# Kernel optimization log

Measured on AMD Instinct MI355X. Metric: run time of the kernel, lower is better.

Reference implementation:

```python
import jax, jax.numpy as jnp
import numpy as np

HEADS = 16
DIM_HEAD = 64
SCALE = DIM_HEAD ** -0.5
EPS = 1e-5


def _vdp_linear(mu, sigma, Wmu, Wsig_raw):
    # y = W x with W ~ N(Wmu, softplus(Wsig_raw)), x ~ N(mu, sigma) (diag covs):
    # Var(y) = (mu^2 + sigma) @ Wsig^T + sigma @ (Wmu^2)^T
    Wsig = jax.nn.softplus(Wsig_raw)
    mu_y = mu @ Wmu.T
    sigma_y = (mu * mu + sigma) @ Wsig.T + sigma @ (Wmu * Wmu).T
    return mu_y, sigma_y


def _vdp_layernorm(mu, sigma, gamma, beta):
    mean = jnp.mean(mu, axis=-1, keepdims=True)
    var = jnp.var(mu, axis=-1, keepdims=True)
    inv = 1.0 / jnp.sqrt(var + EPS)
    mu_y = (mu - mean) * inv * gamma + beta
    # first-order variance propagation through the affine normalization
    sigma_y = sigma * (gamma * gamma) * (inv * inv)
    return mu_y, sigma_y


def _vdp_softmax(mu, sigma):
    p = jax.nn.softmax(mu, axis=-1)
    # diagonal-Jacobian approximation: J_ii = p_i(1-p_i)
    J = p * (1.0 - p)
    return p, (J * J) * sigma


def setup_inputs() -> dict:
    key = jax.random.key(0)
    ks = jax.random.split(key, 6)
    B, N, D = 4, 1024, 1024
    inner = HEADS * DIM_HEAD  # 1024
    w_std = 0.02
    return {
        "mu": jax.random.normal(ks[0], (B, N, D), jnp.float32),
        "sigma": jax.random.uniform(ks[1], (B, N, D), jnp.float32),
        "ln_gamma": jnp.ones((D,), jnp.float32),
        "ln_beta": jnp.zeros((D,), jnp.float32),
        "Wqkv_mu": w_std * jax.random.normal(ks[2], (3 * inner, D), jnp.float32),
        "Wqkv_sigma_raw": -5.0 + 0.1 * jax.random.normal(ks[3], (3 * inner, D), jnp.float32),
        "Wout_mu": w_std * jax.random.normal(ks[4], (D, inner), jnp.float32),
        "Wout_sigma_raw": -5.0 + 0.1 * jax.random.normal(ks[5], (D, inner), jnp.float32),
    }


def reference(mu, sigma, ln_gamma, ln_beta, Wqkv_mu, Wqkv_sigma_raw, Wout_mu, Wout_sigma_raw):
    B, N, D = mu.shape

    mu_n, sigma_n = _vdp_layernorm(mu, sigma, ln_gamma, ln_beta)
    mu_qkv, sigma_qkv = _vdp_linear(mu_n, sigma_n, Wqkv_mu, Wqkv_sigma_raw)

    def split_heads(t):
        q, k, v = jnp.split(t, 3, axis=-1)
        rs = lambda a: a.reshape(B, N, HEADS, DIM_HEAD).transpose(0, 2, 1, 3)
        return rs(q), rs(k), rs(v)

    mu_q, mu_k, mu_v = split_heads(mu_qkv)
    sg_q, sg_k, sg_v = split_heads(sigma_qkv)

    mu_dots = jnp.einsum("bhid,bhjd->bhij", mu_q, mu_k) * SCALE
    sg_dots = jnp.einsum("bhid,bhjd->bhij", sg_q, sg_k) * SCALE

    mu_attn, sg_attn = _vdp_softmax(mu_dots, sg_dots)

    mu_o = jnp.einsum("bhij,bhjd->bhid", mu_attn, mu_v)
    sg_o = jnp.einsum("bhij,bhjd->bhid", sg_attn, sg_v)

    merge = lambda t: t.transpose(0, 2, 1, 3).reshape(B, N, HEADS * DIM_HEAD)
    mu_o, sg_o = merge(mu_o), merge(sg_o)

    return _vdp_linear(mu_o, sg_o, Wout_mu, Wout_sigma_raw)
```

## Files before the change

kernel.cpp:

```cpp
#include <hip/hip_runtime.h>

typedef unsigned short u16;
typedef unsigned int u32;
typedef __bf16 bf16x8 __attribute__((ext_vector_type(8)));
typedef float f32x4 __attribute__((ext_vector_type(4)));
typedef float f32x16 __attribute__((ext_vector_type(16)));

__device__ __forceinline__ float b2f(u16 u) { return __uint_as_float(((u32)u) << 16); }
__device__ __forceinline__ u16 f2b(float f) {
  u32 u = __float_as_uint(f);
  u += 0x7fffu + ((u >> 16) & 1u);
  return (u16)(u >> 16);
}

__device__ __forceinline__ void gll16(const u16* g, u16* l) {
  __builtin_amdgcn_global_load_lds(
      (const __attribute__((address_space(1))) void*)g,
      (__attribute__((address_space(3))) void*)l, 16, 0, 0);
}

__device__ __forceinline__ float4 load4(const void* p, size_t idx, bool f32) {
  if (f32) return *(const float4*)((const float*)p + idx);
  ushort4 u = *(const ushort4*)((const u16*)p + idx);
  return make_float4(b2f(u.x), b2f(u.y), b2f(u.z), b2f(u.w));
}

__global__ __launch_bounds__(256) void detect_kernel(const u16* __restrict__ sig,
                                                     int* __restrict__ flag) {
  __shared__ int cnt;
  if (threadIdx.x == 0) cnt = 0;
  __syncthreads();
  int c = 0;
  for (int i = threadIdx.x; i < 16384; i += 256) {
    u16 v = sig[i];
    c += ((v & 0x7F80u) == 0x7F80u) ? 1 : 0;
  }
  atomicAdd(&cnt, c);
  __syncthreads();
  if (threadIdx.x == 0) *flag = (cnt >= 8) ? 1 : 0;
}

__global__ __launch_bounds__(256) void ln_prep_kernel(
    const int* __restrict__ flag,
    const void* __restrict__ mu, const void* __restrict__ sigma,
    const void* __restrict__ gamma, const void* __restrict__ beta,
    u16* __restrict__ mu_n, u16* __restrict__ a1sg)
{
  __shared__ float ps[4], pq[4];
  const bool f32 = (*flag != 0);
  const int t = threadIdx.x;
  const int wv = t >> 6, lane = t & 63;
  const size_t base = (size_t)blockIdx.x * 1024 + (size_t)t * 4;
  float4 xm = load4(mu, base, f32);
  float4 xs = load4(sigma, base, f32);
  float x0 = xm.x, x1 = xm.y, x2 = xm.z, x3 = xm.w;
  float s0 = xs.x, s1 = xs.y, s2 = xs.z, s3 = xs.w;

  float sv = x0 + x1 + x2 + x3;
  float qv = x0*x0 + x1*x1 + x2*x2 + x3*x3;
  #pragma unroll
  for (int off = 32; off > 0; off >>= 1) {
    sv += __shfl_xor(sv, off, 64);
    qv += __shfl_xor(qv, off, 64);
  }
  if (lane == 0) { ps[wv] = sv; pq[wv] = qv; }
  __syncthreads();
  float sum = ps[0] + ps[1] + ps[2] + ps[3];
  float ssq = pq[0] + pq[1] + pq[2] + pq[3];

  float mean = sum * (1.0f / 1024.0f);
  float var  = ssq * (1.0f / 1024.0f) - mean * mean;
  float inv  = 1.0f / sqrtf(var + 1e-5f);
  float inv2 = inv * inv;

  float4 g4 = load4(gamma, (size_t)t * 4, f32);
  float4 b4 = load4(beta, (size_t)t * 4, f32);

  float m0 = (x0 - mean) * inv * g4.x + b4.x;
  float m1 = (x1 - mean) * inv * g4.y + b4.y;
  float m2 = (x2 - mean) * inv * g4.z + b4.z;
  float m3 = (x3 - mean) * inv * g4.w + b4.w;
  float v0 = s0 * g4.x * g4.x * inv2;
  float v1 = s1 * g4.y * g4.y * inv2;
  float v2 = s2 * g4.z * g4.z * inv2;
  float v3 = s3 * g4.w * g4.w * inv2;

  ushort4 omu = { f2b(m0), f2b(m1), f2b(m2), f2b(m3) };
  ushort4 oa1 = { f2b(m0*m0 + v0), f2b(m1*m1 + v1), f2b(m2*m2 + v2), f2b(m3*m3 + v3) };
  ushort4 osg = { f2b(v0), f2b(v1), f2b(v2), f2b(v3) };
  *(ushort4*)(mu_n + base) = omu;
  size_t r2 = (size_t)blockIdx.x * 2048 + (size_t)t * 4;
  *(ushort4*)(a1sg + r2) = oa1;
  *(ushort4*)(a1sg + r2 + 1024) = osg;
}

__global__ __launch_bounds__(256) void wprep_kernel(
    const int* __restrict__ flag,
    const void* __restrict__ wq_mu, const void* __restrict__ wq_sraw,
    u16* __restrict__ q_bf, u16* __restrict__ q_s2,
    const void* __restrict__ wo_mu, const void* __restrict__ wo_sraw,
    u16* __restrict__ o_bf, u16* __restrict__ o_s2, int nq)
{
  const bool f32 = (*flag != 0);
  size_t idx = ((size_t)blockIdx.x * 256 + threadIdx.x) * 4;
  const void *wmu, *wsr; u16 *obf, *os2;
  if (idx < (size_t)nq) { wmu = wq_mu; wsr = wq_sraw; obf = q_bf; os2 = q_s2; }
  else { idx -= nq; wmu = wo_mu; wsr = wo_sraw; obf = o_bf; os2 = o_s2; }
  int row = (int)(idx >> 10), k = (int)(idx & 1023);
  float4 m4 = load4(wmu, idx, f32);
  float4 s4 = load4(wsr, idx, f32);
  float m[4] = { m4.x, m4.y, m4.z, m4.w };
  float s[4] = { s4.x, s4.y, s4.z, s4.w };
  ushort4 ob, os, oq;
  u16* obp = (u16*)&ob; u16* osp = (u16*)&os; u16* oqp = (u16*)&oq;
  #pragma unroll
  for (int i = 0; i < 4; ++i) {
    float sp = (s[i] > 15.f) ? s[i] : log1pf(__expf(s[i]));
    obp[i] = f2b(m[i]);
    osp[i] = f2b(sp);
    oqp[i] = f2b(m[i] * m[i]);
  }
  *(ushort4*)(obf + idx) = ob;
  size_t r2 = (size_t)row * 2048 + k;
  *(ushort4*)(os2 + r2) = os;
  *(ushort4*)(os2 + r2 + 1024) = oq;
}

template<bool DYN>
__global__ __launch_bounds__(256, 4) void gemm_pair_kernel(
    const u16* __restrict__ A0, const u16* __restrict__ B0, int K0, void* C0, size_t ob0,
    const u16* __restrict__ A1, const u16* __restrict__ B1, int K1, void* C1, size_t ob1,
    int split, int N, const int* __restrict__ flag)
{
  __shared__ u16 lA[128 * 64];
  __shared__ u16 lB[128 * 64];
  const int t = threadIdx.x;
  int bx = blockIdx.x;
  const u16 *A, *B; void* C; size_t obase; int K;
  if (bx < split) { A = A0; B = B0; K = K0; C = C0; obase = ob0; }
  else { bx -= split; A = A1; B = B1; K = K1; C = C1; obase = ob1; }

  const int n0 = bx * 128, m0 = blockIdx.y * 128;
  const int lane = t & 63, wave = t >> 6;
  const int wr = (wave >> 1) * 64, wc = (wave & 1) * 64;
  const int m31 = lane & 31, h5 = lane >> 5;
  const int mx = m31 & 7;

  const int srow = t >> 3;
  const int gseg = (t & 7) ^ (srow & 7);

  f32x16 acc[2][2];
  #pragma unroll
  for (int i = 0; i < 2; ++i)
    #pragma unroll
    for (int j = 0; j < 2; ++j)
      #pragma unroll
      for (int r = 0; r < 16; ++r) acc[i][j][r] = 0.f;

  for (int k0 = 0; k0 < K; k0 += 64) {
    __syncthreads();
    #pragma unroll
    for (int rep = 0; rep < 4; ++rep) {
      gll16(A + (size_t)(m0 + srow + rep * 32) * K + k0 + gseg * 8,
            lA + rep * 2048 + wave * 512);
      gll16(B + (size_t)(n0 + srow + rep * 32) * K + k0 + gseg * 8,
            lB + rep * 2048 + wave * 512);
    }
    __syncthreads();
    #pragma unroll
    for (int ks = 0; ks < 4; ++ks) {
      const int seg = ks * 2 + h5;
      bf16x8 af[2], bfr[2];
      #pragma unroll
      for (int tm = 0; tm < 2; ++tm)
        af[tm] = *(const bf16x8*)&lA[(wr + tm * 32 + m31) * 64 + (seg ^ mx) * 8];
      #pragma unroll
      for (int tn = 0; tn < 2; ++tn)
        bfr[tn] = *(const bf16x8*)&lB[(wc + tn * 32 + m31) * 64 + (seg ^ mx) * 8];
      #pragma unroll
      for (int tm = 0; tm < 2; ++tm)
        #pragma unroll
        for (int tn = 0; tn < 2; ++tn)
          acc[tm][tn] = __builtin_amdgcn_mfma_f32_32x32x16_bf16(af[tm], bfr[tn], acc[tm][tn], 0, 0, 0);
    }
  }

  const bool of32 = DYN && (*flag != 0);
  #pragma unroll
  for (int tm = 0; tm < 2; ++tm)
    #pragma unroll
    for (int tn = 0; tn < 2; ++tn) {
      int colb = n0 + wc + tn * 32 + m31;
      #pragma unroll
      for (int r = 0; r < 16; ++r) {
        int row = m0 + wr + tm * 32 + (r & 3) + 8 * (r >> 2) + 4 * h5;
        float v = acc[tm][tn][r];
        size_t off = obase + (size_t)row * N + colb;
        if (DYN) {
          if (of32) ((float*)C)[off] = v;
          else      ((u16*)C)[off] = f2b(v);
        } else {
          ((u16*)C)[off] = f2b(v);
        }
      }
    }
}

__global__ __launch_bounds__(256) void attn_pass1(
    const u16* __restrict__ qkv_mu, float* __restrict__ invl)
{
  __shared__ u16 lK[128 * 72];
  const int t = threadIdx.x;
  const int wv = t >> 6, lane = t & 63;
  const int ml = lane & 15, qd = lane >> 4;
  const int bh = blockIdx.y;
  const int b = bh >> 4, h = bh & 15;
  const size_t rowbase = (size_t)b * 1024 * 3072;
  const int i0 = blockIdx.x * 64;
  const int qcol = h * 64, kcol = 1024 + h * 64;
  const int qrow = wv * 16;

  bf16x8 aQm[2];
  #pragma unroll
  for (int ks = 0; ks < 2; ++ks)
    aQm[ks] = *(const bf16x8*)(qkv_mu + rowbase +
        (size_t)(i0 + qrow + ml) * 3072 + qcol + ks * 32 + qd * 8);

  float lsum[4] = {0.f, 0.f, 0.f, 0.f};

  for (int j0 = 0; j0 < 1024; j0 += 128) {
    __syncthreads();
    #pragma unroll
    for (int rep = 0; rep < 4; ++rep) {
      int c = t + rep * 256;
      int row = c >> 3, seg = c & 7;
      *(uint4*)&lK[row * 72 + seg * 8] =
          *(const uint4*)(qkv_mu + rowbase + (size_t)(j0 + row) * 3072 + kcol + seg * 8);
    }
    __syncthreads();
    #pragma unroll
    for (int tj = 0; tj < 8; ++tj) {
      bf16x8 b0 = *(const bf16x8*)&lK[(tj * 16 + ml) * 72 + qd * 8];
      bf16x8 b1 = *(const bf16x8*)&lK[(tj * 16 + ml) * 72 + 32 + qd * 8];
      f32x4 s = (f32x4){0.f, 0.f, 0.f, 0.f};
      s = __builtin_amdgcn_mfma_f32_16x16x32_bf16(aQm[0], b0, s, 0, 0, 0);
      s = __builtin_amdgcn_mfma_f32_16x16x32_bf16(aQm[1], b1, s, 0, 0, 0);
      #pragma unroll
      for (int r = 0; r < 4; ++r) lsum[r] += __expf(s[r] * 0.125f);
    }
  }
  #pragma unroll
  for (int r = 0; r < 4; ++r) {
    float l = lsum[r];
    #pragma unroll
    for (int xo = 1; xo < 16; xo <<= 1) l += __shfl_xor(l, xo, 64);
    if (ml == 0)
      invl[(size_t)bh * 1024 + i0 + qrow + qd * 4 + r] = 1.0f / l;
  }
}

__global__ __launch_bounds__(512, 4) void attn_pass2(
    const u16* __restrict__ qkv_mu, const u16* __restrict__ qkv_sg,
    const float* __restrict__ invl,
    u16* __restrict__ o_mu, u16* __restrict__ a1sgo)
{
  __shared__ u16 lKW[128 * 72];
  __shared__ u16 lV[128 * 72];
  __shared__ u16 lP[128 * 72];
  __shared__ u16 lW[128 * 72];

  const int t = threadIdx.x;
  const int wv = t >> 6, lane = t & 63;
  const int ml = lane & 15, qd = lane >> 4;
  const int bh = blockIdx.y;
  const int b = bh >> 4, h = bh & 15;
  const size_t rowbase = (size_t)b * 1024 * 3072;
  const int i0 = blockIdx.x * 128;
  const int qcol = h * 64, kcol = 1024 + h * 64, vcol = 2048 + h * 64;
  const int qrow = wv * 16;

  bf16x8 aQm[2], aQs[2];
  #pragma unroll
  for (int ks = 0; ks < 2; ++ks) {
    size_t ga = rowbase + (size_t)(i0 + qrow + ml) * 3072 + qcol + ks * 32 + qd * 8;
    aQm[ks] = *(const bf16x8*)(qkv_mu + ga);
    aQs[ks] = *(const bf16x8*)(qkv_sg + ga);
  }

  float lacc[4];
  #pragma unroll
  for (int r = 0; r < 4; ++r)
    lacc[r] = invl[(size_t)bh * 1024 + i0 + qrow + qd * 4 + r];

  f32x4 accm[4], accs[4];
  #pragma unroll
  for (int tj = 0; tj < 4; ++tj) {
    accm[tj] = (f32x4){0.f, 0.f, 0.f, 0.f};
    accs[tj] = (f32x4){0.f, 0.f, 0.f, 0.f};
  }

  for (int j0 = 0; j0 < 1024; j0 += 64) {
    __syncthreads();
    #pragma unroll
    for (int rep = 0; rep < 2; ++rep) {
      int c = t + rep * 512;
      int row = c >> 3, seg = c & 7;
      const u16* src = (row < 64) ? qkv_mu : qkv_sg;
      int rr = row & 63;
      *(uint4*)&lKW[row * 72 + seg * 8] =
          *(const uint4*)(src + rowbase + (size_t)(j0 + rr) * 3072 + kcol + seg * 8);
    }
    {
      int buf = t >> 8, rem = t & 255;
      int db = rem >> 4, tb = rem & 15;
      const u16* src = buf ? qkv_sg : qkv_mu;
      ushort4 vals[4];
      #pragma unroll
      for (int i = 0; i < 4; ++i)
        vals[i] = *(const ushort4*)(src + rowbase + (size_t)(j0 + tb * 4 + i) * 3072 + vcol + db * 4);
      #pragma unroll
      for (int k = 0; k < 4; ++k) {
        ushort4 o;
        u16* op = (u16*)&o;
        const u16* v0 = (const u16*)&vals[0];
        const u16* v1 = (const u16*)&vals[1];
        const u16* v2 = (const u16*)&vals[2];
        const u16* v3 = (const u16*)&vals[3];
        op[0] = v0[k]; op[1] = v1[k]; op[2] = v2[k]; op[3] = v3[k];
        *(ushort4*)&lV[(buf * 64 + db * 4 + k) * 72 + tb * 4] = o;
      }
    }
    __syncthreads();

    f32x4 sm[4], ss[4];
    #pragma unroll
    for (int tj = 0; tj < 4; ++tj) {
      bf16x8 bm0 = *(const bf16x8*)&lKW[(tj * 16 + ml) * 72 + qd * 8];
      bf16x8 bm1 = *(const bf16x8*)&lKW[(tj * 16 + ml) * 72 + 32 + qd * 8];
      bf16x8 bs0 = *(const bf16x8*)&lKW[(64 + tj * 16 + ml) * 72 + qd * 8];
      bf16x8 bs1 = *(const bf16x8*)&lKW[(64 + tj * 16 + ml) * 72 + 32 + qd * 8];
      f32x4 s = (f32x4){0.f, 0.f, 0.f, 0.f};
      s = __builtin_amdgcn_mfma_f32_16x16x32_bf16(aQm[0], bm0, s, 0, 0, 0);
      s = __builtin_amdgcn_mfma_f32_16x16x32_bf16(aQm[1], bm1, s, 0, 0, 0);
      sm[tj] = s;
      f32x4 s2 = (f32x4){0.f, 0.f, 0.f, 0.f};
      s2 = __builtin_amdgcn_mfma_f32_16x16x32_bf16(aQs[0], bs0, s2, 0, 0, 0);
      s2 = __builtin_amdgcn_mfma_f32_16x16x32_bf16(aQs[1], bs1, s2, 0, 0, 0);
      ss[tj] = s2;
    }

    #pragma unroll
    for (int tj = 0; tj < 4; ++tj)
      #pragma unroll
      for (int r = 0; r < 4; ++r) {
        float p = __expf(sm[tj][r] * 0.125f) * lacc[r];
        float jp = p * (1.0f - p);
        float w = jp * jp * (ss[tj][r] * 0.125f);
        int row = qrow + qd * 4 + r;
        lP[row * 72 + tj * 16 + ml] = f2b(p);
        lW[row * 72 + tj * 16 + ml] = f2b(w);
      }
    __syncthreads();

    bf16x8 ap[2], aw[2];
    #pragma unroll
    for (int ks = 0; ks < 2; ++ks) {
      ap[ks] = *(const bf16x8*)&lP[(qrow + ml) * 72 + ks * 32 + qd * 8];
      aw[ks] = *(const bf16x8*)&lW[(qrow + ml) * 72 + ks * 32 + qd * 8];
    }
    #pragma unroll
    for (int tj = 0; tj < 4; ++tj) {
      bf16x8 vm0 = *(const bf16x8*)&lV[(tj * 16 + ml) * 72 + qd * 8];
      bf16x8 vm1 = *(const bf16x8*)&lV[(tj * 16 + ml) * 72 + 32 + qd * 8];
      bf16x8 vs0 = *(const bf16x8*)&lV[(64 + tj * 16 + ml) * 72 + qd * 8];
      bf16x8 vs1 = *(const bf16x8*)&lV[(64 + tj * 16 + ml) * 72 + 32 + qd * 8];
      accm[tj] = __builtin_amdgcn_mfma_f32_16x16x32_bf16(ap[0], vm0, accm[tj], 0, 0, 0);
      accm[tj] = __builtin_amdgcn_mfma_f32_16x16x32_bf16(ap[1], vm1, accm[tj], 0, 0, 0);
      accs[tj] = __builtin_amdgcn_mfma_f32_16x16x32_bf16(aw[0], vs0, accs[tj], 0, 0, 0);
      accs[tj] = __builtin_amdgcn_mfma_f32_16x16x32_bf16(aw[1], vs1, accs[tj], 0, 0, 0);
    }
  }

  #pragma unroll
  for (int tj = 0; tj < 4; ++tj)
    #pragma unroll
    for (int r = 0; r < 4; ++r) {
      int row = i0 + qrow + qd * 4 + r;
      int col = h * 64 + tj * 16 + ml;
      size_t rowg = (size_t)b * 1024 + row;
      float om = accm[tj][r], os = accs[tj][r];
      o_mu[rowg * 1024 + col] = f2b(om);
      size_t r2 = rowg * 2048 + col;
      a1sgo[r2] = f2b(fmaf(om, om, os));
      a1sgo[r2 + 1024] = f2b(os);
    }
}

extern "C" void kernel_launch(void* const* d_in, const int* in_sizes, int n_in,
                              void* d_out, int out_size, void* d_ws, size_t ws_size,
                              hipStream_t stream)
{
  (void)in_sizes; (void)n_in; (void)out_size; (void)ws_size;
  const void* mu        = d_in[0];
  const void* sigma     = d_in[1];
  const void* gamma     = d_in[2];
  const void* beta      = d_in[3];
  const void* wqkv_mu   = d_in[4];
  const void* wqkv_sraw = d_in[5];
  const void* wout_mu   = d_in[6];
  const void* wout_sraw = d_in[7];

  u16* ws = (u16*)d_ws;
  const size_t R = 4096;
  u16* mu_n   = ws;
  u16* a1sg   = mu_n + R * 1024;
  u16* wq_bf  = a1sg + R * 2048;
  u16* wqs2   = wq_bf + 3072 * 1024;
  u16* wo_bf  = wqs2 + 3072 * 2048;
  u16* wos2   = wo_bf + 1024 * 1024;
  u16* mu_qkv = wos2 + 1024 * 2048;
  u16* sg_qkv = mu_qkv + R * 3072;
  int* flag   = (int*)(sg_qkv + R * 3072);
  float* invl = (float*)(flag + 16);

  u16* mu_o  = mu_n;
  u16* a1sgo = a1sg;

  detect_kernel<<<1, 256, 0, stream>>>((const u16*)sigma, flag);
  ln_prep_kernel<<<4096, 256, 0, stream>>>(flag, mu, sigma, gamma, beta, mu_n, a1sg);
  wprep_kernel<<<(4 * 1024 * 1024) / 1024, 256, 0, stream>>>(
      flag, wqkv_mu, wqkv_sraw, wq_bf, wqs2,
      wout_mu, wout_sraw, wo_bf, wos2, 3072 * 1024);

  gemm_pair_kernel<false><<<dim3(48, 32), 256, 0, stream>>>(
      mu_n, wq_bf, 1024, mu_qkv, 0,
      a1sg, wqs2, 2048, sg_qkv, 0,
      24, 3072, nullptr);

  attn_pass1<<<dim3(16, 64), 256, 0, stream>>>(mu_qkv, invl);
  attn_pass2<<<dim3(8, 64), 512, 0, stream>>>(mu_qkv, sg_qkv, invl, mu_o, a1sgo);

  gemm_pair_kernel<true><<<dim3(16, 32), 256, 0, stream>>>(
      mu_o, wo_bf, 1024, d_out, 0,
      a1sgo, wos2, 2048, d_out, R * 1024,
      8, 1024, flag);
}
```

Baseline: 399.3 us.

## Add 256x256-tile 8-wave pipelined GEMM for the QKV projection pair

```diff
diff --git a/kernel.cpp b/kernel.cpp
--- a/kernel.cpp
+++ b/kernel.cpp
@@ -204,6 +204,156 @@
         }
       }
     }
+}
+
+#define SB __builtin_amdgcn_sched_barrier(0)
+#define BARRIER do { SB; __builtin_amdgcn_s_barrier(); SB; } while (0)
+
+__global__ __launch_bounds__(512, 2) void gemm8_pair_kernel(
+    const u16* __restrict__ A0, const u16* __restrict__ B0, int K0, u16* __restrict__ C0,
+    const u16* __restrict__ A1, const u16* __restrict__ B1, int K1, u16* __restrict__ C1,
+    int split, int N)
+{
+  __shared__ u16 lA[2 * 2 * 128 * 64];
+  __shared__ u16 lB[2 * 2 * 128 * 64];
+  const int t = threadIdx.x;
+  int bx = blockIdx.x;
+  const u16 *A, *B; u16* C; int K;
+  if (bx < split) { A = A0; B = B0; K = K0; C = C0; }
+  else { bx -= split; A = A1; B = B1; K = K1; C = C1; }
+  const int NT = K >> 6;
+  const int n0 = bx * 256, m0 = blockIdx.y * 256;
+  const int lane = t & 63, wave = t >> 6;
+  const int wm = wave >> 2, wn = wave & 3;
+  const int ml = lane & 15, qd = lane >> 4, mx = ml & 7;
+
+  auto stg = [&](const u16* __restrict__ X, int row0, int k0, u16* ldsHalf) {
+    #pragma unroll
+    for (int j = 0; j < 2; ++j) {
+      int r = (wave * 2 + j) * 8 + (lane >> 3);
+      int seg = (lane & 7) ^ ((lane >> 3) & 7);
+      gll16(X + (size_t)(row0 + r) * K + k0 + seg * 8,
+            ldsHalf + (wave * 2 + j) * 512);
+    }
+  };
+
+  const u16* rdA = lA + (wm * 128 + ml) * 64;
+  const u16* rdB = lB + ((wn >> 1) * 128 + (wn & 1) * 64 + ml) * 64;
+
+  f32x4 acc[8][4];
+  #pragma unroll
+  for (int i = 0; i < 8; ++i)
+    #pragma unroll
+    for (int j = 0; j < 4; ++j)
+      acc[i][j] = (f32x4){0.f, 0.f, 0.f, 0.f};
+
+  bf16x8 fa[4][2];
+  bf16x8 fb[2][2][2];
+
+  stg(A, m0,       0,  lA);
+  stg(A, m0 + 128, 0,  lA + 8192);
+  stg(B, n0,       0,  lB);
+  stg(B, n0 + 128, 0,  lB + 8192);
+  if (NT > 1) {
+    stg(B, n0,       64, lB + 16384);
+    stg(B, n0 + 128, 64, lB + 16384 + 8192);
+  }
+  SB;
+  asm volatile("s_waitcnt vmcnt(4)" ::: "memory");
+  BARRIER;
+
+  for (int T = 0; T < NT; ++T) {
+    const int bo  = (T & 1) * 16384;
+    const int bon = bo ^ 16384;
+    const int kn  = (T + 1) * 64;
+    const int kn2 = (T + 2) * 64;
+
+    #pragma unroll
+    for (int i = 0; i < 4; ++i)
+      #pragma unroll
+      for (int ks = 0; ks < 2; ++ks)
+        fa[i][ks] = *(const bf16x8*)&rdA[bo + i * 1024 + ((ks * 4 + qd) ^ mx) * 8];
+    #pragma unroll
+    for (int j = 0; j < 2; ++j)
+      #pragma unroll
+      for (int ks = 0; ks < 2; ++ks)
+        fb[0][j][ks] = *(const bf16x8*)&rdB[bo + j * 1024 + ((ks * 4 + qd) ^ mx) * 8];
+    if (T + 1 < NT) stg(A, m0, kn, lA + bon);
+    BARRIER;
+    __builtin_amdgcn_s_setprio(1);
+    #pragma unroll
+    for (int i = 0; i < 4; ++i)
+      #pragma unroll
+      for (int j = 0; j < 2; ++j)
+        #pragma unroll
+        for (int ks = 0; ks < 2; ++ks)
+          acc[i][j] = __builtin_amdgcn_mfma_f32_16x16x32_bf16(fa[i][ks], fb[0][j][ks], acc[i][j], 0, 0, 0);
+    __builtin_amdgcn_s_setprio(0);
+    BARRIER;
+
+    #pragma unroll
+    for (int j = 0; j < 2; ++j)
+      #pragma unroll
+      for (int ks = 0; ks < 2; ++ks)
+        fb[1][j][ks] = *(const bf16x8*)&rdB[bo + (2 + j) * 1024 + ((ks * 4 + qd) ^ mx) * 8];
+    if (T + 1 < NT) stg(A, m0 + 128, kn, lA + bon + 8192);
+    BARRIER;
+    __builtin_amdgcn_s_setprio(1);
+    #pragma unroll
+    for (int i = 0; i < 4; ++i)
+      #pragma unroll
+      for (int j = 0; j < 2; ++j)
+        #pragma unroll
+        for (int ks = 0; ks < 2; ++ks)
+          acc[i][2 + j] = __builtin_amdgcn_mfma_f32_16x16x32_bf16(fa[i][ks], fb[1][j][ks], acc[i][2 + j], 0, 0, 0);
+    __builtin_amdgcn_s_setprio(0);
+    BARRIER;
+
+    #pragma unroll
+    for (int i = 0; i < 4; ++i)
+      #pragma unroll
+      for (int ks = 0; ks < 2; ++ks)
+        fa[i][ks] = *(const bf16x8*)&rdA[bo + (4 + i) * 1024 + ((ks * 4 + qd) ^ mx) * 8];
+    if (T + 2 < NT) stg(B, n0, kn2, lB + bo);
+    BARRIER;
+    __builtin_amdgcn_s_setprio(1);
+    #pragma unroll
+    for (int i = 0; i < 4; ++i)
+      #pragma unroll
+      for (int j = 0; j < 2; ++j)
+        #pragma unroll
+        for (int ks = 0; ks < 2; ++ks)
+          acc[4 + i][2 + j] = __builtin_amdgcn_mfma_f32_16x16x32_bf16(fa[i][ks], fb[1][j][ks], acc[4 + i][2 + j], 0, 0, 0);
+    __builtin_amdgcn_s_setprio(0);
+    BARRIER;
+
+    if (T + 2 < NT) stg(B, n0 + 128, kn2, lB + bo + 8192);
+    BARRIER;
+    __builtin_amdgcn_s_setprio(1);
+    #pragma unroll
+    for (int i = 0; i < 4; ++i)
+      #pragma unroll
+      for (int j = 0; j < 2; ++j)
+        #pragma unroll
+        for (int ks = 0; ks < 2; ++ks)
+          acc[4 + i][j] = __builtin_amdgcn_mfma_f32_16x16x32_bf16(fa[i][ks], fb[0][j][ks], acc[4 + i][j], 0, 0, 0);
+    __builtin_amdgcn_s_setprio(0);
+    SB;
+    if (T + 2 < NT) asm volatile("s_waitcnt vmcnt(4)" ::: "memory");
+    else            asm volatile("s_waitcnt vmcnt(0)" ::: "memory");
+    BARRIER;
+  }
+
+  #pragma unroll
+  for (int mf = 0; mf < 8; ++mf)
+    #pragma unroll
+    for (int nf = 0; nf < 4; ++nf)
+      #pragma unroll
+      for (int r = 0; r < 4; ++r) {
+        int row = m0 + wm * 128 + mf * 16 + qd * 4 + r;
+        int col = n0 + wn * 64 + nf * 16 + ml;
+        C[(size_t)row * N + col] = f2b(acc[mf][nf][r]);
+      }
 }
 
 __global__ __launch_bounds__(256) void attn_pass1(
@@ -432,10 +582,10 @@
       flag, wqkv_mu, wqkv_sraw, wq_bf, wqs2,
       wout_mu, wout_sraw, wo_bf, wos2, 3072 * 1024);
 
-  gemm_pair_kernel<false><<<dim3(48, 32), 256, 0, stream>>>(
-      mu_n, wq_bf, 1024, mu_qkv, 0,
-      a1sg, wqs2, 2048, sg_qkv, 0,
-      24, 3072, nullptr);
+  gemm8_pair_kernel<<<dim3(24, 16), 512, 0, stream>>>(
+      mu_n, wq_bf, 1024, mu_qkv,
+      a1sg, wqs2, 2048, sg_qkv,
+      12, 3072);
 
   attn_pass1<<<dim3(16, 64), 256, 0, stream>>>(mu_qkv, invl);
   attn_pass2<<<dim3(8, 64), 512, 0, stream>>>(mu_qkv, sg_qkv, invl, mu_o, a1sgo);
```

Result: no change. 405.4 us (+1.5%).
